# Kernel optimization log

Measured on AMD Instinct MI355X. Metric: run time of the kernel, lower is better.

## Reference

```python
import jax, jax.numpy as jnp
import numpy as np

K = 4096          # num_embeddings
D = 256           # embedding_dim
COMMIT = 0.25     # commitment_cost


def setup_inputs() -> dict:
    key = jax.random.key(0)
    k1, k2 = jax.random.split(key)
    z = jax.random.normal(k1, (16, D, 32, 32), dtype=jnp.float32)
    # codebook init: uniform(-1/K, 1/K) as in the torch module
    emb = jax.random.uniform(k2, (K, D), dtype=jnp.float32,
                             minval=-1.0 / K, maxval=1.0 / K)
    return {"z": z, "emb": emb}


def reference(z, emb):
    B, Dm, H, W = z.shape
    # (B, D, H, W) -> (B*H*W, D)
    z_flat = jnp.transpose(z, (0, 2, 3, 1)).reshape(-1, Dm)
    # squared L2 distances to every codebook vector: (N, K)
    distances = (jnp.sum(z_flat * z_flat, axis=1, keepdims=True)
                 + jnp.sum(emb * emb, axis=1)
                 - 2.0 * jnp.matmul(z_flat, emb.T))
    encoding_indices = jnp.argmin(distances, axis=1)            # (N,)
    encodings = jax.nn.one_hot(encoding_indices, emb.shape[0],
                               dtype=z.dtype)                   # (N, K)
    quantized = jnp.take(emb, encoding_indices, axis=0)         # == encodings @ emb

    sg = jax.lax.stop_gradient
    e_latent_loss = jnp.mean((sg(quantized) - z_flat) ** 2)
    q_latent_loss = jnp.mean((quantized - sg(z_flat)) ** 2)
    loss = q_latent_loss + COMMIT * e_latent_loss

    avg_probs = jnp.mean(encodings, axis=0)
    perplexity = jnp.exp(-jnp.sum(avg_probs * jnp.log(avg_probs + 1e-10)))

    # straight-through estimator
    quantized = z_flat + sg(quantized - z_flat)
    # NOTE: faithful to source: torch does .view(B, D, H, W) on the (N, D)
    # flat tensor WITHOUT permuting back -- a plain reshape, replicated here.
    quantized = quantized.reshape(B, Dm, H, W)
    return quantized, loss, perplexity, encodings
```

## Files before the change

kernel.cpp:

```cpp
#include <hip/hip_runtime.h>

#define NN 16384
#define KK 4096
#define DD 256

typedef __attribute__((ext_vector_type(8))) short short8;
typedef __attribute__((ext_vector_type(4))) float f32x4;

static __device__ __forceinline__ unsigned short f2bf(float f) {
  unsigned u = __float_as_uint(f);
  return (unsigned short)((u + 0x7FFFu + ((u >> 16) & 1u)) >> 16);
}

static __device__ __forceinline__ unsigned int mono(float f) {
  unsigned u = __float_as_uint(f);
  return (u & 0x80000000u) ? ~u : (u | 0x80000000u);
}

__global__ __launch_bounds__(256) void vq_prep(
    const float* __restrict__ z, const float* __restrict__ emb,
    unsigned short* __restrict__ zb, unsigned short* __restrict__ eb,
    float* __restrict__ e2g, unsigned long long* __restrict__ keys,
    unsigned int* __restrict__ counts, float* __restrict__ lossacc) {
  __shared__ unsigned short t[64][72];
  const int tid = threadIdx.x;
  const int bx = blockIdx.x;

  if (bx < 1024) {
    const int b = bx >> 6, rem = bx & 63, dt = rem >> 4, ht = rem & 15;
    const float* src = z + (long)b * 262144 + (long)dt * 65536 + ht * 64;
    #pragma unroll
    for (int p = 0; p < 16; ++p) {
      int idx = p * 256 + tid;
      int dl = idx >> 6, hl = idx & 63;
      t[hl][dl] = f2bf(src[dl * 1024 + hl]);
    }
    __syncthreads();
    unsigned short* dst = zb + ((long)b * 1024 + (long)ht * 64) * DD + dt * 64;
    #pragma unroll
    for (int p = 0; p < 2; ++p) {
      int idx = p * 256 + tid;
      int hl = idx >> 3, c8 = idx & 7;
      short8 v = *reinterpret_cast<const short8*>(&t[hl][c8 * 8]);
      *reinterpret_cast<short8*>(&dst[(long)hl * DD + c8 * 8]) = v;
    }
  } else if (bx < 2048) {
    const int wid = tid >> 6, lane = tid & 63;
    const int row = (bx - 1024) * 4 + wid;
    float4 v = *reinterpret_cast<const float4*>(&emb[row * DD + lane * 4]);
    ushort4 w;
    w.x = f2bf(v.x); w.y = f2bf(v.y); w.z = f2bf(v.z); w.w = f2bf(v.w);
    *reinterpret_cast<ushort4*>(&eb[row * DD + lane * 4]) = w;
    float s = v.x * v.x + v.y * v.y + v.z * v.z + v.w * v.w;
    #pragma unroll
    for (int o = 1; o < 64; o <<= 1) s += __shfl_xor(s, o);
    if (lane == 0) e2g[row] = s;
  } else {
    int tt = (bx - 2048) * 256 + tid;
    #pragma unroll
    for (int i = 0; i < 8; ++i) keys[tt * 8 + i] = ~0ull;
    counts[tt * 2] = 0u;
    counts[tt * 2 + 1] = 0u;
    if (tt == 0) lossacc[0] = 0.f;
  }
}

__global__ __launch_bounds__(256) void vq_gemm(
    const unsigned short* __restrict__ eb, const unsigned short* __restrict__ zb,
    const float* __restrict__ e2g, unsigned long long* __restrict__ keys,
    float* __restrict__ enc) {
  __shared__ unsigned short At[128 * 64];
  __shared__ unsigned short Bt[128 * 64];
  __shared__ float e2s[128];
  __shared__ unsigned long long wkey[2][128];

  const int tid = threadIdx.x;
  const int bm = blockIdx.x;
  const int bn = blockIdx.y;
  const int lane = tid & 63, wid = tid >> 6;
  const int wm = wid >> 1, wn = wid & 1;
  const int l16 = lane & 15, g4 = lane >> 4;

  if (tid < 128) {
    e2s[tid] = e2g[bm * 128 + tid];
    wkey[0][tid] = ~0ull;
    wkey[1][tid] = ~0ull;
  }

  const long abase = (long)bm * 128 * DD;
  const long bbase = (long)bn * 128 * DD;

  f32x4 acc[4][4];
  #pragma unroll
  for (int mi = 0; mi < 4; ++mi)
    #pragma unroll
    for (int ni = 0; ni < 4; ++ni) acc[mi][ni] = (f32x4){0.f, 0.f, 0.f, 0.f};

  for (int kt = 0; kt < 4; ++kt) {
    __syncthreads();
    {
      const int lr = lane >> 3, lc = (lane & 7) * 8;
      #pragma unroll
      for (int c = 0; c < 4; ++c) {
        const int row0 = wid * 32 + c * 8;
        const unsigned short* ga =
            eb + abase + (long)(row0 + lr) * DD + kt * 64 + lc;
        __builtin_amdgcn_global_load_lds(
            (const __attribute__((address_space(1))) void*)ga,
            (__attribute__((address_space(3))) void*)&At[row0 * 64], 16, 0, 0);
        const unsigned short* gb =
            zb + bbase + (long)(row0 + lr) * DD + kt * 64 + lc;
        __builtin_amdgcn_global_load_lds(
            (const __attribute__((address_space(1))) void*)gb,
            (__attribute__((address_space(3))) void*)&Bt[row0 * 64], 16, 0, 0);
      }
    }
    __syncthreads();

    #pragma unroll
    for (int kk = 0; kk < 2; ++kk) {
      short8 a[4], b[4];
      #pragma unroll
      for (int mi = 0; mi < 4; ++mi)
        a[mi] = *reinterpret_cast<const short8*>(
            &At[(wm * 64 + mi * 16 + l16) * 64 + kk * 32 + g4 * 8]);
      #pragma unroll
      for (int ni = 0; ni < 4; ++ni)
        b[ni] = *reinterpret_cast<const short8*>(
            &Bt[(wn * 64 + ni * 16 + l16) * 64 + kk * 32 + g4 * 8]);
      #pragma unroll
      for (int mi = 0; mi < 4; ++mi)
        #pragma unroll
        for (int ni = 0; ni < 4; ++ni)
          acc[mi][ni] = __builtin_amdgcn_mfma_f32_16x16x32_bf16(
              a[mi], b[ni], acc[mi][ni], 0, 0, 0);
    }
  }

  #pragma unroll
  for (int ni = 0; ni < 4; ++ni) {
    float bv = INFINITY;
    int bi = 0;
    #pragma unroll
    for (int mi = 0; mi < 4; ++mi) {
      #pragma unroll
      for (int r = 0; r < 4; ++r) {
        int krow = wm * 64 + mi * 16 + g4 * 4 + r;
        float s = fmaf(-2.0f, acc[mi][ni][r], e2s[krow]);
        if (s < bv) { bv = s; bi = bm * 128 + krow; }
      }
    }
    unsigned long long key =
        ((unsigned long long)mono(bv) << 32) | (unsigned)bi;
    unsigned long long o;
    o = __shfl_xor(key, 16); if (o < key) key = o;
    o = __shfl_xor(key, 32); if (o < key) key = o;
    if (g4 == 0) wkey[wm][wn * 64 + ni * 16 + l16] = key;
  }
  __syncthreads();
  if (tid < 128) {
    unsigned long long k0 = wkey[0][tid], k1 = wkey[1][tid];
    atomicMin(&keys[(long)bn * 128 + tid], k0 < k1 ? k0 : k1);
  }

  {
    const long base = ((long)(bm * 128 + bn)) * 16384;
    const f32x4 zero4 = (f32x4){0.f, 0.f, 0.f, 0.f};
    #pragma unroll
    for (int i = 0; i < 16; ++i)
      *reinterpret_cast<f32x4*>(&enc[base + (long)(i * 256 + tid) * 4]) = zero4;
  }
}

__global__ __launch_bounds__(256) void vq_finish(
    const float* __restrict__ z, const float* __restrict__ emb,
    const unsigned long long* __restrict__ keys, unsigned int* __restrict__ counts,
    float* __restrict__ lossacc, float* __restrict__ outq, float* __restrict__ enc) {
  __shared__ float ztile[64][257];
  __shared__ int sidx[64];
  __shared__ float wsum[4];

  const int tid = threadIdx.x;
  const int n0 = blockIdx.x * 64;
  const long zbase = (long)(n0 >> 10) * 262144 + (long)(n0 & 1023);

  {
    int n4 = (tid & 15) << 2;
    int dl = tid >> 4;
    for (int p = 0; p < 16; ++p) {
      int d = p * 16 + dl;
      float4 v = *reinterpret_cast<const float4*>(&z[zbase + (long)d * 1024 + n4]);
      ztile[n4 + 0][d] = v.x;
      ztile[n4 + 1][d] = v.y;
      ztile[n4 + 2][d] = v.z;
      ztile[n4 + 3][d] = v.w;
    }
  }
  if (tid < 64) {
    int n = n0 + tid;
    int idx = (int)(keys[n] & 0xFFFFFFFFULL);
    sidx[tid] = idx;
    atomicAdd(&counts[idx], 1u);
    enc[(long)n * KK + idx] = 1.0f;
  }
  __syncthreads();

  float lacc = 0.f;
  const int d = tid;
  for (int nl = 0; nl < 64; ++nl) {
    int idx = sidx[nl];
    float e = emb[idx * DD + d];
    float zz = ztile[nl][d];
    float df = e - zz;
    lacc += df * df;
    outq[(long)(n0 + nl) * DD + d] = zz + (e - zz);
  }
  #pragma unroll
  for (int o = 1; o < 64; o <<= 1) lacc += __shfl_xor(lacc, o);
  if ((tid & 63) == 0) wsum[tid >> 6] = lacc;
  __syncthreads();
  if (tid == 0) atomicAdd(lossacc, wsum[0] + wsum[1] + wsum[2] + wsum[3]);
}

__global__ void vq_scalars(const unsigned int* __restrict__ counts,
                           const float* __restrict__ lossacc,
                           float* __restrict__ outs) {
  __shared__ double sh[256];
  int t = threadIdx.x;
  double ent = 0.0;
  for (int k = t; k < KK; k += 256) {
    double p = (double)counts[k] / (double)NN;
    ent += p * log(p + 1e-10);
  }
  sh[t] = ent;
  __syncthreads();
  for (int s = 128; s > 0; s >>= 1) {
    if (t < s) sh[t] += sh[t + s];
    __syncthreads();
  }
  if (t == 0) {
    outs[0] = lossacc[0] * 1.25f / ((float)NN * (float)DD);
    outs[1] = (float)exp(-sh[0]);
  }
}

extern "C" void kernel_launch(void* const* d_in, const int* in_sizes, int n_in,
                              void* d_out, int out_size, void* d_ws, size_t ws_size,
                              hipStream_t stream) {
  const float* z = (const float*)d_in[0];
  const float* emb = (const float*)d_in[1];
  float* out = (float*)d_out;
  float* outq = out;
  float* outs = out + 4194304;
  float* enc = out + 4194306;

  char* ws = (char*)d_ws;
  unsigned short* zb = (unsigned short*)ws;
  unsigned short* eb = (unsigned short*)(ws + 8388608);
  float* e2g = (float*)(ws + 10485760);
  unsigned long long* keys = (unsigned long long*)(ws + 10502144);
  unsigned int* counts = (unsigned int*)(ws + 10633216);
  float* lossacc = (float*)(ws + 10649600);

  vq_prep<<<2056, 256, 0, stream>>>(z, emb, zb, eb, e2g, keys, counts, lossacc);
  vq_gemm<<<dim3(32, 128), 256, 0, stream>>>(eb, zb, e2g, keys, enc);
  vq_finish<<<NN / 64, 256, 0, stream>>>(z, emb, keys, counts, lossacc, outq, enc);
  vq_scalars<<<1, 256, 0, stream>>>(counts, lossacc, outs);
}
```

Before: 352.5 us.

## Double-buffer GEMM LDS staging and fold scalar reduction into finish kernel

```diff
diff --git a/kernel.cpp b/kernel.cpp
--- a/kernel.cpp
+++ b/kernel.cpp
@@ -21,7 +21,8 @@
     const float* __restrict__ z, const float* __restrict__ emb,
     unsigned short* __restrict__ zb, unsigned short* __restrict__ eb,
     float* __restrict__ e2g, unsigned long long* __restrict__ keys,
-    unsigned int* __restrict__ counts, float* __restrict__ lossacc) {
+    unsigned int* __restrict__ counts, float* __restrict__ lossacc,
+    unsigned int* __restrict__ donecnt) {
   __shared__ unsigned short t[64][72];
   const int tid = threadIdx.x;
   const int bx = blockIdx.x;
@@ -61,7 +62,7 @@
     for (int i = 0; i < 8; ++i) keys[tt * 8 + i] = ~0ull;
     counts[tt * 2] = 0u;
     counts[tt * 2 + 1] = 0u;
-    if (tt == 0) lossacc[0] = 0.f;
+    if (tt == 0) { lossacc[0] = 0.f; donecnt[0] = 0u; }
   }
 }
 
@@ -69,8 +70,8 @@
     const unsigned short* __restrict__ eb, const unsigned short* __restrict__ zb,
     const float* __restrict__ e2g, unsigned long long* __restrict__ keys,
     float* __restrict__ enc) {
-  __shared__ unsigned short At[128 * 64];
-  __shared__ unsigned short Bt[128 * 64];
+  __shared__ unsigned short At[2][128 * 64];
+  __shared__ unsigned short Bt[2][128 * 64];
   __shared__ float e2s[128];
   __shared__ unsigned long long wkey[2][128];
 
@@ -89,6 +90,24 @@
 
   const long abase = (long)bm * 128 * DD;
   const long bbase = (long)bn * 128 * DD;
+  const int lr = lane >> 3, lc = (lane & 7) * 8;
+
+  auto stage = [&](int buf, int kt) {
+    #pragma unroll
+    for (int c = 0; c < 4; ++c) {
+      const int row0 = wid * 32 + c * 8;
+      const unsigned short* ga =
+          eb + abase + (long)(row0 + lr) * DD + kt * 64 + lc;
+      __builtin_amdgcn_global_load_lds(
+          (const __attribute__((address_space(1))) void*)ga,
+          (__attribute__((address_space(3))) void*)&At[buf][row0 * 64], 16, 0, 0);
+      const unsigned short* gb =
+          zb + bbase + (long)(row0 + lr) * DD + kt * 64 + lc;
+      __builtin_amdgcn_global_load_lds(
+          (const __attribute__((address_space(1))) void*)gb,
+          (__attribute__((address_space(3))) void*)&Bt[buf][row0 * 64], 16, 0, 0);
+    }
+  };
 
   f32x4 acc[4][4];
   #pragma unroll
@@ -96,26 +115,19 @@
     #pragma unroll
     for (int ni = 0; ni < 4; ++ni) acc[mi][ni] = (f32x4){0.f, 0.f, 0.f, 0.f};
 
+  stage(0, 0);
+  #pragma unroll
   for (int kt = 0; kt < 4; ++kt) {
-    __syncthreads();
-    {
-      const int lr = lane >> 3, lc = (lane & 7) * 8;
-      #pragma unroll
-      for (int c = 0; c < 4; ++c) {
-        const int row0 = wid * 32 + c * 8;
-        const unsigned short* ga =
-            eb + abase + (long)(row0 + lr) * DD + kt * 64 + lc;
-        __builtin_amdgcn_global_load_lds(
-            (const __attribute__((address_space(1))) void*)ga,
-            (__attribute__((address_space(3))) void*)&At[row0 * 64], 16, 0, 0);
-        const unsigned short* gb =
-            zb + bbase + (long)(row0 + lr) * DD + kt * 64 + lc;
-        __builtin_amdgcn_global_load_lds(
-            (const __attribute__((address_space(1))) void*)gb,
-            (__attribute__((address_space(3))) void*)&Bt[row0 * 64], 16, 0, 0);
-      }
-    }
-    __syncthreads();
+    const int cur = kt & 1;
+    asm volatile("s_waitcnt lgkmcnt(0)" ::: "memory");
+    __builtin_amdgcn_s_barrier();
+    if (kt < 3) {
+      stage(cur ^ 1, kt + 1);
+      asm volatile("s_waitcnt vmcnt(8)" ::: "memory");
+    } else {
+      asm volatile("s_waitcnt vmcnt(0)" ::: "memory");
+    }
+    __builtin_amdgcn_s_barrier();
 
     #pragma unroll
     for (int kk = 0; kk < 2; ++kk) {
@@ -123,11 +135,11 @@
       #pragma unroll
       for (int mi = 0; mi < 4; ++mi)
         a[mi] = *reinterpret_cast<const short8*>(
-            &At[(wm * 64 + mi * 16 + l16) * 64 + kk * 32 + g4 * 8]);
+            &At[cur][(wm * 64 + mi * 16 + l16) * 64 + kk * 32 + g4 * 8]);
       #pragma unroll
       for (int ni = 0; ni < 4; ++ni)
         b[ni] = *reinterpret_cast<const short8*>(
-            &Bt[(wn * 64 + ni * 16 + l16) * 64 + kk * 32 + g4 * 8]);
+            &Bt[cur][(wn * 64 + ni * 16 + l16) * 64 + kk * 32 + g4 * 8]);
       #pragma unroll
       for (int mi = 0; mi < 4; ++mi)
         #pragma unroll
@@ -175,10 +187,13 @@
 __global__ __launch_bounds__(256) void vq_finish(
     const float* __restrict__ z, const float* __restrict__ emb,
     const unsigned long long* __restrict__ keys, unsigned int* __restrict__ counts,
-    float* __restrict__ lossacc, float* __restrict__ outq, float* __restrict__ enc) {
+    float* __restrict__ lossacc, unsigned int* __restrict__ donecnt,
+    float* __restrict__ outq, float* __restrict__ enc, float* __restrict__ outs) {
   __shared__ float ztile[64][257];
   __shared__ int sidx[64];
   __shared__ float wsum[4];
+  __shared__ double sh[256];
+  __shared__ unsigned int lastflag;
 
   const int tid = threadIdx.x;
   const int n0 = blockIdx.x * 64;
@@ -207,6 +222,7 @@
 
   float lacc = 0.f;
   const int d = tid;
+  #pragma unroll 4
   for (int nl = 0; nl < 64; ++nl) {
     int idx = sidx[nl];
     float e = emb[idx * DD + d];
@@ -220,27 +236,28 @@
   if ((tid & 63) == 0) wsum[tid >> 6] = lacc;
   __syncthreads();
   if (tid == 0) atomicAdd(lossacc, wsum[0] + wsum[1] + wsum[2] + wsum[3]);
-}
-
-__global__ void vq_scalars(const unsigned int* __restrict__ counts,
-                           const float* __restrict__ lossacc,
-                           float* __restrict__ outs) {
-  __shared__ double sh[256];
-  int t = threadIdx.x;
-  double ent = 0.0;
-  for (int k = t; k < KK; k += 256) {
-    double p = (double)counts[k] / (double)NN;
-    ent += p * log(p + 1e-10);
-  }
-  sh[t] = ent;
-  __syncthreads();
-  for (int s = 128; s > 0; s >>= 1) {
-    if (t < s) sh[t] += sh[t + s];
+
+  __threadfence();
+  if (tid == 0) lastflag = (atomicAdd(donecnt, 1u) == (unsigned)(NN / 64 - 1));
+  __syncthreads();
+  if (lastflag) {
+    double ent = 0.0;
+    for (int k = tid; k < KK; k += 256) {
+      unsigned c = atomicAdd(&counts[k], 0u);
+      double p = (double)c / (double)NN;
+      ent += p * log(p + 1e-10);
+    }
+    sh[tid] = ent;
     __syncthreads();
-  }
-  if (t == 0) {
-    outs[0] = lossacc[0] * 1.25f / ((float)NN * (float)DD);
-    outs[1] = (float)exp(-sh[0]);
+    for (int s = 128; s > 0; s >>= 1) {
+      if (tid < s) sh[tid] += sh[tid + s];
+      __syncthreads();
+    }
+    if (tid == 0) {
+      float la = atomicAdd(lossacc, 0.f);
+      outs[0] = la * 1.25f / ((float)NN * (float)DD);
+      outs[1] = (float)exp(-sh[0]);
+    }
   }
 }
 
@@ -261,9 +278,11 @@
   unsigned long long* keys = (unsigned long long*)(ws + 10502144);
   unsigned int* counts = (unsigned int*)(ws + 10633216);
   float* lossacc = (float*)(ws + 10649600);
-
-  vq_prep<<<2056, 256, 0, stream>>>(z, emb, zb, eb, e2g, keys, counts, lossacc);
+  unsigned int* donecnt = (unsigned int*)(ws + 10649604);
+
+  vq_prep<<<2056, 256, 0, stream>>>(z, emb, zb, eb, e2g, keys, counts,
+                                    lossacc, donecnt);
   vq_gemm<<<dim3(32, 128), 256, 0, stream>>>(eb, zb, e2g, keys, enc);
-  vq_finish<<<NN / 64, 256, 0, stream>>>(z, emb, keys, counts, lossacc, outq, enc);
-  vq_scalars<<<1, 256, 0, stream>>>(counts, lossacc, outs);
-}
+  vq_finish<<<NN / 64, 256, 0, stream>>>(z, emb, keys, counts, lossacc,
+                                         donecnt, outq, enc, outs);
+}
```

Result: slower. 382.2 us (+8.4%).

## Derive loss from argmin distance keys and drop the z re-read in finish

Applied to the files above, without the earlier changes.

```diff
diff --git a/kernel.cpp b/kernel.cpp
--- a/kernel.cpp
+++ b/kernel.cpp
@@ -23,19 +23,28 @@
     float* __restrict__ e2g, unsigned long long* __restrict__ keys,
     unsigned int* __restrict__ counts, float* __restrict__ lossacc) {
   __shared__ unsigned short t[64][72];
+  __shared__ float zws[4];
   const int tid = threadIdx.x;
   const int bx = blockIdx.x;
 
   if (bx < 1024) {
     const int b = bx >> 6, rem = bx & 63, dt = rem >> 4, ht = rem & 15;
     const float* src = z + (long)b * 262144 + (long)dt * 65536 + ht * 64;
+    float sq = 0.f;
     #pragma unroll
     for (int p = 0; p < 16; ++p) {
       int idx = p * 256 + tid;
       int dl = idx >> 6, hl = idx & 63;
-      t[hl][dl] = f2bf(src[dl * 1024 + hl]);
-    }
-    __syncthreads();
+      float val = src[dl * 1024 + hl];
+      t[hl][dl] = f2bf(val);
+      sq += val * val;
+    }
+    #pragma unroll
+    for (int o = 1; o < 64; o <<= 1) sq += __shfl_xor(sq, o);
+    if ((tid & 63) == 0) zws[tid >> 6] = sq;
+    __syncthreads();
+    if (tid == 0)
+      atomicAdd(lossacc, zws[0] + zws[1] + zws[2] + zws[3]);
     unsigned short* dst = zb + ((long)b * 1024 + (long)ht * 64) * DD + dt * 64;
     #pragma unroll
     for (int p = 0; p < 2; ++p) {
@@ -173,53 +182,37 @@
 }
 
 __global__ __launch_bounds__(256) void vq_finish(
-    const float* __restrict__ z, const float* __restrict__ emb,
-    const unsigned long long* __restrict__ keys, unsigned int* __restrict__ counts,
-    float* __restrict__ lossacc, float* __restrict__ outq, float* __restrict__ enc) {
-  __shared__ float ztile[64][257];
+    const float* __restrict__ emb, const unsigned long long* __restrict__ keys,
+    unsigned int* __restrict__ counts, float* __restrict__ lossacc,
+    float* __restrict__ outq, float* __restrict__ enc) {
   __shared__ int sidx[64];
-  __shared__ float wsum[4];
-
   const int tid = threadIdx.x;
   const int n0 = blockIdx.x * 64;
-  const long zbase = (long)(n0 >> 10) * 262144 + (long)(n0 & 1023);
-
-  {
-    int n4 = (tid & 15) << 2;
-    int dl = tid >> 4;
-    for (int p = 0; p < 16; ++p) {
-      int d = p * 16 + dl;
-      float4 v = *reinterpret_cast<const float4*>(&z[zbase + (long)d * 1024 + n4]);
-      ztile[n4 + 0][d] = v.x;
-      ztile[n4 + 1][d] = v.y;
-      ztile[n4 + 2][d] = v.z;
-      ztile[n4 + 3][d] = v.w;
-    }
-  }
+
   if (tid < 64) {
     int n = n0 + tid;
-    int idx = (int)(keys[n] & 0xFFFFFFFFULL);
+    unsigned long long k = keys[n];
+    int idx = (int)(k & 0xFFFFFFFFULL);
     sidx[tid] = idx;
     atomicAdd(&counts[idx], 1u);
     enc[(long)n * KK + idx] = 1.0f;
+    unsigned m = (unsigned)(k >> 32);
+    float best = (m & 0x80000000u) ? __uint_as_float(m ^ 0x80000000u)
+                                   : __uint_as_float(~m);
+    #pragma unroll
+    for (int o = 1; o < 64; o <<= 1) best += __shfl_xor(best, o);
+    if (tid == 0) atomicAdd(lossacc, best);
   }
   __syncthreads();
 
-  float lacc = 0.f;
-  const int d = tid;
-  for (int nl = 0; nl < 64; ++nl) {
-    int idx = sidx[nl];
-    float e = emb[idx * DD + d];
-    float zz = ztile[nl][d];
-    float df = e - zz;
-    lacc += df * df;
-    outq[(long)(n0 + nl) * DD + d] = zz + (e - zz);
-  }
-  #pragma unroll
-  for (int o = 1; o < 64; o <<= 1) lacc += __shfl_xor(lacc, o);
-  if ((tid & 63) == 0) wsum[tid >> 6] = lacc;
-  __syncthreads();
-  if (tid == 0) atomicAdd(lossacc, wsum[0] + wsum[1] + wsum[2] + wsum[3]);
+  const float4* emb4 = reinterpret_cast<const float4*>(emb);
+  float4* outq4 = reinterpret_cast<float4*>(outq);
+  const int nl0 = tid >> 6, c = tid & 63;
+  #pragma unroll 4
+  for (int p = 0; p < 16; ++p) {
+    int nl = p * 4 + nl0;
+    outq4[(long)(n0 + nl) * 64 + c] = emb4[(long)sidx[nl] * 64 + c];
+  }
 }
 
 __global__ void vq_scalars(const unsigned int* __restrict__ counts,
@@ -264,6 +257,6 @@
 
   vq_prep<<<2056, 256, 0, stream>>>(z, emb, zb, eb, e2g, keys, counts, lossacc);
   vq_gemm<<<dim3(32, 128), 256, 0, stream>>>(eb, zb, e2g, keys, enc);
-  vq_finish<<<NN / 64, 256, 0, stream>>>(z, emb, keys, counts, lossacc, outq, enc);
+  vq_finish<<<NN / 64, 256, 0, stream>>>(emb, keys, counts, lossacc, outq, enc);
   vq_scalars<<<1, 256, 0, stream>>>(counts, lossacc, outs);
 }
```

New measurement: 357.3 us. About the same (+1.3%).
